# Performance work log

Measured on AMD Instinct MI355X. Metric: run time of the kernel, lower is better.

Reference implementation:

```python
import jax, jax.numpy as jnp
import numpy as np

NUM_HEADS = 16
EMBED_DIM = 1024
LN_EPS = 1e-5


def setup_inputs() -> dict:
    key = jax.random.key(0)
    ks = jax.random.split(key, 9)
    B, S, D = 4, 1024, EMBED_DIM
    return {
        "query": jax.random.normal(ks[0], (B, S, D), dtype=jnp.float32),
        "key": jax.random.normal(ks[1], (B, S, D), dtype=jnp.float32),
        "value": jax.random.normal(ks[2], (B, S, D), dtype=jnp.float32),
        "W_query": 0.01 * jax.random.normal(ks[3], (D, D), dtype=jnp.float32),
        "W_key": 0.01 * jax.random.normal(ks[4], (D, D), dtype=jnp.float32),
        "W_value": 0.01 * jax.random.normal(ks[5], (D, D), dtype=jnp.float32),
        "W_output": 0.01 * jax.random.normal(ks[6], (D, D), dtype=jnp.float32),
        "ln_gamma": jnp.ones((D,), dtype=jnp.float32),
        "ln_beta": jnp.zeros((D,), dtype=jnp.float32),
        "mask": 1,
    }


def _split_heads(x):
    # [B,S,D] -> [H,B,S,d]; torch split(dim=-1)+stack(dim=0) gives head h = cols h*d:(h+1)*d
    B, S, D = x.shape
    d = D // NUM_HEADS
    return jnp.moveaxis(x.reshape(B, S, NUM_HEADS, d), 2, 0)


def reference(query, key, value, W_query, W_key, W_value, W_output, ln_gamma, ln_beta, mask):
    B, S, D = query.shape
    d = D // NUM_HEADS
    q = _split_heads(query @ W_query)   # [H,B,S,d]
    k = _split_heads(key @ W_key)       # [H,B,S,d]
    v = _split_heads(value @ W_value)   # [H,B,S,d]
    scale = jnp.asarray(np.sqrt(d), dtype=q.dtype)
    scores = jnp.einsum("hbqd,hbkd->hbqk", q, k) / scale  # [H,B,S,S]
    attn = jax.nn.softmax(scores, axis=-1)
    if mask:
        # post-hoc causal: zero strict upper triangle, then renormalize rows
        tri = jnp.tril(jnp.ones((S, S), dtype=bool))
        attn = jnp.where(tri, attn, 0.0)
        attn = attn / jnp.sum(attn, axis=-1, keepdims=True)
    ws = jnp.einsum("hbqk,hbkd->hbqd", attn, v)            # [H,B,S,d]
    concat = jnp.moveaxis(ws, 0, 2).reshape(B, S, D)       # [B,S,D]
    out = concat @ W_output + query                        # residual
    mu = jnp.mean(out, axis=-1, keepdims=True)
    var = jnp.var(out, axis=-1, keepdims=True)
    out = (out - mu) / jnp.sqrt(var + LN_EPS) * ln_gamma + ln_beta
    return out, attn
```

## Files before the change

kernel.cpp:

```cpp
#include <hip/hip_runtime.h>
#include <hip/hip_bf16.h>

#define Bn   4
#define Sn   1024
#define Dn   1024
#define Hn   16
#define dHn  64
#define HB   (Hn * Bn)
#define MROWS (Bn * Sn)
#define QNE  ((size_t)Bn * Sn * Dn)

typedef __attribute__((ext_vector_type(8))) short bf16x8;
typedef __attribute__((ext_vector_type(4))) float f32x4;

__device__ __forceinline__ ushort f2bf(float x) {
  union { float f; unsigned u; } v; v.f = x;
  unsigned r = v.u + 0x7FFF + ((v.u >> 16) & 1);
  return (ushort)(r >> 16);
}
__device__ __forceinline__ float bf2f(ushort u) {
  union { unsigned u; float f; } v; v.u = ((unsigned)u) << 16; return v.f;
}

__device__ __forceinline__ void load_lds16(const void* g, void* l) {
  __builtin_amdgcn_global_load_lds(
      (const __attribute__((address_space(1))) unsigned int*)g,
      (__attribute__((address_space(3))) unsigned int*)l, 16, 0, 0);
}

__global__ __launch_bounds__(256) void cast3_kernel(
    const float* __restrict__ q, const float* __restrict__ k,
    const float* __restrict__ v, ushort* __restrict__ outb) {
  const float* in = blockIdx.y == 0 ? q : (blockIdx.y == 1 ? k : v);
  ushort* out = outb + (size_t)blockIdx.y * QNE;
  int idx = blockIdx.x * 256 + threadIdx.x;
  float4 x = *(const float4*)&in[(size_t)idx * 4];
  ushort4 o;
  o.x = f2bf(x.x); o.y = f2bf(x.y); o.z = f2bf(x.z); o.w = f2bf(x.w);
  *(ushort4*)&out[(size_t)idx * 4] = o;
}

__global__ __launch_bounds__(256) void transpose4_kernel(
    const float* __restrict__ Wq, const float* __restrict__ Wk,
    const float* __restrict__ Wv, const float* __restrict__ Wo,
    ushort* __restrict__ WTb) {
  const int z = blockIdx.z;
  const float* W = z == 0 ? Wq : (z == 1 ? Wk : (z == 2 ? Wv : Wo));
  ushort* WT = WTb + (size_t)z * Dn * Dn;
  __shared__ ushort T[64 * 72];
  const int k0 = blockIdx.y * 64, n0 = blockIdx.x * 64;
  const int t = threadIdx.x;
  const int r = t >> 4, c4 = (t & 15) * 4;
#pragma unroll
  for (int i = 0; i < 4; ++i) {
    int row = r + i * 16;
    float4 v = *(const float4*)&W[(size_t)(k0 + row) * Dn + n0 + c4];
    T[(c4 + 0) * 72 + row] = f2bf(v.x);
    T[(c4 + 1) * 72 + row] = f2bf(v.y);
    T[(c4 + 2) * 72 + row] = f2bf(v.z);
    T[(c4 + 3) * 72 + row] = f2bf(v.w);
  }
  __syncthreads();
#pragma unroll
  for (int i = 0; i < 2; ++i) {
    int c = t + i * 256;
    int n = c >> 3, kg = (c & 7) * 8;
    *(ulonglong2*)&WT[(size_t)(n0 + n) * Dn + k0 + kg] =
        *(const ulonglong2*)&T[n * 72 + kg];
  }
}

__global__ __launch_bounds__(256, 3) void qkv_gemm(
    const ushort* __restrict__ Ab, const ushort* __restrict__ Bb,
    ushort* __restrict__ Cb) {
  const int z = blockIdx.z;
  const ushort* A  = Ab + (size_t)z * QNE;
  const ushort* Bt = Bb + (size_t)z * Dn * Dn;
  ushort* C        = Cb + (size_t)z * QNE;
  const int M = MROWS, N = Dn, K = Dn;

  __shared__ ushort lds[17408];
  ushort* As = lds;
  ushort* Bs = lds + 4096;
  const int t = threadIdx.x;
  const int w = t >> 6, lane = t & 63;
  const int wr = (w >> 1) * 64, wc = (w & 1) * 64;
  const int l16 = lane & 15, quad = lane >> 4;
  const int m0 = blockIdx.y * 128, n0 = blockIdx.x * 128;
  const int srow = (lane >> 2);
  const int scol = (lane & 3) * 8;
  f32x4 acc[4][4] = {};
  for (int k0 = 0; k0 < K; k0 += 32) {
#pragma unroll
    for (int c = 0; c < 2; ++c) {
      int row = w * 32 + c * 16 + srow;
      load_lds16(&A[(size_t)(m0 + row) * K + k0 + scol],
                 &As[(size_t)w * 1024 + c * 512]);
      load_lds16(&Bt[(size_t)(n0 + row) * K + k0 + scol],
                 &Bs[(size_t)w * 1024 + c * 512]);
    }
    __syncthreads();
    bf16x8 af[4], bfr[4];
#pragma unroll
    for (int mi = 0; mi < 4; ++mi)
      af[mi] = *(const bf16x8*)&As[(wr + mi * 16 + l16) * 32 + quad * 8];
#pragma unroll
    for (int ni = 0; ni < 4; ++ni)
      bfr[ni] = *(const bf16x8*)&Bs[(wc + ni * 16 + l16) * 32 + quad * 8];
#pragma unroll
    for (int mi = 0; mi < 4; ++mi)
#pragma unroll
      for (int ni = 0; ni < 4; ++ni)
        acc[mi][ni] = __builtin_amdgcn_mfma_f32_16x16x32_bf16(
            af[mi], bfr[ni], acc[mi][ni], 0, 0, 0);
    __syncthreads();
  }
  if (z == 2) {
#pragma unroll
    for (int mi = 0; mi < 4; ++mi) {
      int mb = m0 + wr + mi * 16 + quad * 4;
      int b = mb >> 10, s = mb & 1023;
#pragma unroll
      for (int ni = 0; ni < 4; ++ni) {
        int n = n0 + wc + ni * 16 + l16;
        ushort4 o;
        o.x = f2bf(acc[mi][ni][0]);
        o.y = f2bf(acc[mi][ni][1]);
        o.z = f2bf(acc[mi][ni][2]);
        o.w = f2bf(acc[mi][ni][3]);
        *(ushort4*)&C[((size_t)b * N + n) * Sn + s] = o;
      }
    }
  } else {
    ushort* Cs = lds;
#pragma unroll
    for (int mi = 0; mi < 4; ++mi)
#pragma unroll
      for (int ni = 0; ni < 4; ++ni) {
        int col = wc + ni * 16 + l16;
#pragma unroll
        for (int r = 0; r < 4; ++r)
          Cs[(wr + mi * 16 + quad * 4 + r) * 136 + col] = f2bf(acc[mi][ni][r]);
      }
    __syncthreads();
#pragma unroll
    for (int i = 0; i < 8; ++i) {
      int c = t + i * 256;
      int row = c >> 4, cg = (c & 15) * 8;
      *(ulonglong2*)&C[(size_t)(m0 + row) * N + n0 + cg] =
          *(const ulonglong2*)&Cs[row * 136 + cg];
    }
  }
}

__global__ __launch_bounds__(256) void gemm_out(
    const ushort* __restrict__ A, const ushort* __restrict__ Bt,
    const float* __restrict__ resid, float* __restrict__ C,
    int M, int N, int K) {
  __shared__ ushort lds[8192];
  ushort* As = lds;
  ushort* Bs = lds + 4096;
  const int t = threadIdx.x;
  const int w = t >> 6, lane = t & 63;
  const int wr = (w >> 1) * 64, wc = (w & 1) * 64;
  const int l16 = lane & 15, quad = lane >> 4;
  const int m0 = blockIdx.y * 128, n0 = blockIdx.x * 128;
  const int srow = (lane >> 2);
  const int scol = (lane & 3) * 8;
  f32x4 acc[4][4] = {};
  for (int k0 = 0; k0 < K; k0 += 32) {
#pragma unroll
    for (int c = 0; c < 2; ++c) {
      int row = w * 32 + c * 16 + srow;
      load_lds16(&A[(size_t)(m0 + row) * K + k0 + scol],
                 &As[(size_t)w * 1024 + c * 512]);
      load_lds16(&Bt[(size_t)(n0 + row) * K + k0 + scol],
                 &Bs[(size_t)w * 1024 + c * 512]);
    }
    __syncthreads();
    bf16x8 af[4], bfr[4];
#pragma unroll
    for (int mi = 0; mi < 4; ++mi)
      af[mi] = *(const bf16x8*)&As[(wr + mi * 16 + l16) * 32 + quad * 8];
#pragma unroll
    for (int ni = 0; ni < 4; ++ni)
      bfr[ni] = *(const bf16x8*)&Bs[(wc + ni * 16 + l16) * 32 + quad * 8];
#pragma unroll
    for (int mi = 0; mi < 4; ++mi)
#pragma unroll
      for (int ni = 0; ni < 4; ++ni)
        acc[mi][ni] = __builtin_amdgcn_mfma_f32_16x16x32_bf16(
            af[mi], bfr[ni], acc[mi][ni], 0, 0, 0);
    __syncthreads();
  }
#pragma unroll
  for (int mi = 0; mi < 4; ++mi)
#pragma unroll
    for (int ni = 0; ni < 4; ++ni) {
      int n = n0 + wc + ni * 16 + l16;
#pragma unroll
      for (int r = 0; r < 4; ++r) {
        int m = m0 + wr + mi * 16 + quad * 4 + r;
        float v = acc[mi][ni][r];
        v += resid[(size_t)m * N + n];
        C[(size_t)m * N + n] = v;
      }
    }
}

__global__ __launch_bounds__(256, 3) void attn_fused(
    const ushort* __restrict__ Qp, const ushort* __restrict__ Kp,
    const ushort* __restrict__ Vt, float* __restrict__ attn,
    ushort* __restrict__ Cc) {
  const int hb = blockIdx.x, qt = blockIdx.y;
  const int h = hb >> 2, b = hb & 3;
  const int q0 = qt * 64;
  const int nkt = (qt >> 1) + 1;

  __shared__ ushort Ks[128 * 72];
  __shared__ ushort Vs[64 * 136];
  __shared__ ushort Ps[64 * 136];

  const int t = threadIdx.x;
  const int w = t >> 6, lane = t & 63;
  const int l16 = lane & 15, quad = lane >> 4;

  for (int ktz = nkt; ktz < 8; ++ktz) {
    const int k0 = ktz * 128;
#pragma unroll
    for (int i = 0; i < 4; ++i) {
      int cc = t + i * 256;
      int row = cc >> 4, cg = (cc & 15) * 8;
      float* dst = &attn[((size_t)hb * Sn + q0 + row) * Sn + k0 + cg];
      *(float4*)&dst[0] = make_float4(0.f, 0.f, 0.f, 0.f);
      *(float4*)&dst[4] = make_float4(0.f, 0.f, 0.f, 0.f);
    }
  }

  bf16x8 aq[2];
#pragma unroll
  for (int ks = 0; ks < 2; ++ks)
    aq[ks] = *(const bf16x8*)&Qp[((size_t)b * Sn + q0 + w * 16 + l16) * Dn +
                                 h * dHn + ks * 32 + quad * 8];

  float m_run[4], l_run[4];
#pragma unroll
  for (int r = 0; r < 4; ++r) { m_run[r] = -3e38f; l_run[r] = 0.f; }

  for (int kt = 0; kt < nkt; ++kt) {
    const int k0 = kt * 128;
#pragma unroll
    for (int i = 0; i < 4; ++i) {
      int cc = t + i * 256;
      int row = cc >> 3, cg = (cc & 7) * 8;
      *(ulonglong2*)&Ks[row * 72 + cg] =
          *(const ulonglong2*)&Kp[((size_t)b * Sn + k0 + row) * Dn + h * dHn + cg];
    }
    __syncthreads();
    f32x4 s[8];
#pragma unroll
    for (int ni = 0; ni < 8; ++ni) {
      f32x4 a = {};
#pragma unroll
      for (int ks = 0; ks < 2; ++ks) {
        bf16x8 bk = *(const bf16x8*)&Ks[(ni * 16 + l16) * 72 + ks * 32 + quad * 8];
        a = __builtin_amdgcn_mfma_f32_16x16x32_bf16(aq[ks], bk, a, 0, 0, 0);
      }
      s[ni] = a;
    }
    float tmax[4] = {-3e38f, -3e38f, -3e38f, -3e38f};
#pragma unroll
    for (int ni = 0; ni < 8; ++ni)
#pragma unroll
      for (int r = 0; r < 4; ++r) {
        int kg = k0 + ni * 16 + l16;
        int qg = q0 + w * 16 + quad * 4 + r;
        float v = (kg <= qg) ? s[ni][r] * 0.125f : -3e38f;
        s[ni][r] = v;
        tmax[r] = fmaxf(tmax[r], v);
      }
#pragma unroll
    for (int d = 1; d < 16; d <<= 1)
#pragma unroll
      for (int r = 0; r < 4; ++r)
        tmax[r] = fmaxf(tmax[r], __shfl_xor(tmax[r], d));
    float mnew[4], tsum[4] = {0.f, 0.f, 0.f, 0.f};
#pragma unroll
    for (int r = 0; r < 4; ++r) mnew[r] = fmaxf(m_run[r], tmax[r]);
#pragma unroll
    for (int ni = 0; ni < 8; ++ni)
#pragma unroll
      for (int r = 0; r < 4; ++r) tsum[r] += __expf(s[ni][r] - mnew[r]);
#pragma unroll
    for (int d = 1; d < 16; d <<= 1)
#pragma unroll
      for (int r = 0; r < 4; ++r) tsum[r] += __shfl_xor(tsum[r], d);
#pragma unroll
    for (int r = 0; r < 4; ++r) {
      l_run[r] = l_run[r] * __expf(m_run[r] - mnew[r]) + tsum[r];
      m_run[r] = mnew[r];
    }
    __syncthreads();
  }
  float inv_l[4];
#pragma unroll
  for (int r = 0; r < 4; ++r) inv_l[r] = 1.0f / l_run[r];

  f32x4 acc_o[4] = {};
  for (int kt = 0; kt < nkt; ++kt) {
    const int k0 = kt * 128;
#pragma unroll
    for (int i = 0; i < 4; ++i) {
      int cc = t + i * 256;
      int row = cc >> 3, cg = (cc & 7) * 8;
      *(ulonglong2*)&Ks[row * 72 + cg] =
          *(const ulonglong2*)&Kp[((size_t)b * Sn + k0 + row) * Dn + h * dHn + cg];
    }
#pragma unroll
    for (int i = 0; i < 4; ++i) {
      int cc = t + i * 256;
      int row = cc >> 4, cg = (cc & 15) * 8;
      *(ulonglong2*)&Vs[row * 136 + cg] =
          *(const ulonglong2*)&Vt[((size_t)b * Dn + h * dHn + row) * Sn + k0 + cg];
    }
    __syncthreads();
    f32x4 s[8];
#pragma unroll
    for (int ni = 0; ni < 8; ++ni) {
      f32x4 a = {};
#pragma unroll
      for (int ks = 0; ks < 2; ++ks) {
        bf16x8 bk = *(const bf16x8*)&Ks[(ni * 16 + l16) * 72 + ks * 32 + quad * 8];
        a = __builtin_amdgcn_mfma_f32_16x16x32_bf16(aq[ks], bk, a, 0, 0, 0);
      }
      s[ni] = a;
    }
#pragma unroll
    for (int ni = 0; ni < 8; ++ni)
#pragma unroll
      for (int r = 0; r < 4; ++r) {
        int kg = k0 + ni * 16 + l16;
        int qg = q0 + w * 16 + quad * 4 + r;
        float v = (kg <= qg) ? s[ni][r] * 0.125f : -3e38f;
        float p = __expf(v - m_run[r]) * inv_l[r];
        Ps[(w * 16 + quad * 4 + r) * 136 + ni * 16 + l16] = f2bf(p);
      }
#pragma unroll
    for (int ks = 0; ks < 4; ++ks) {
      bf16x8 ap = *(const bf16x8*)&Ps[(w * 16 + l16) * 136 + ks * 32 + quad * 8];
#pragma unroll
      for (int ni = 0; ni < 4; ++ni) {
        bf16x8 bv = *(const bf16x8*)&Vs[(ni * 16 + l16) * 136 + ks * 32 + quad * 8];
        acc_o[ni] = __builtin_amdgcn_mfma_f32_16x16x32_bf16(ap, bv, acc_o[ni], 0, 0, 0);
      }
    }
    __syncthreads();
#pragma unroll
    for (int i = 0; i < 4; ++i) {
      int cc = t + i * 256;
      int row = cc >> 4, cg = (cc & 15) * 8;
      bf16x8 pv = *(const bf16x8*)&Ps[row * 136 + cg];
      float* dst = &attn[((size_t)hb * Sn + q0 + row) * Sn + k0 + cg];
      *(float4*)&dst[0] = make_float4(bf2f((ushort)pv[0]), bf2f((ushort)pv[1]),
                                      bf2f((ushort)pv[2]), bf2f((ushort)pv[3]));
      *(float4*)&dst[4] = make_float4(bf2f((ushort)pv[4]), bf2f((ushort)pv[5]),
                                      bf2f((ushort)pv[6]), bf2f((ushort)pv[7]));
    }
  }
#pragma unroll
  for (int ni = 0; ni < 4; ++ni)
#pragma unroll
    for (int r = 0; r < 4; ++r) {
      int q = q0 + w * 16 + quad * 4 + r;
      int j = ni * 16 + l16;
      Cc[((size_t)b * Sn + q) * Dn + h * dHn + j] = f2bf(acc_o[ni][r]);
    }
}

__global__ __launch_bounds__(256) void ln_kernel(
    float* __restrict__ out, const float* __restrict__ gamma,
    const float* __restrict__ beta) {
  const int row = blockIdx.x;
  float* p = out + (size_t)row * Dn;
  const int t = threadIdx.x;
  float v[4];
  float s = 0.f, s2 = 0.f;
#pragma unroll
  for (int i = 0; i < 4; ++i) {
    v[i] = p[t + i * 256];
    s += v[i];
    s2 += v[i] * v[i];
  }
  __shared__ float r1[256], r2[256];
  r1[t] = s; r2[t] = s2;
  __syncthreads();
  for (int st = 128; st > 0; st >>= 1) {
    if (t < st) { r1[t] += r1[t + st]; r2[t] += r2[t + st]; }
    __syncthreads();
  }
  const float mu  = r1[0] * (1.0f / Dn);
  const float var = r2[0] * (1.0f / Dn) - mu * mu;
  const float rstd = rsqrtf(var + 1e-5f);
#pragma unroll
  for (int i = 0; i < 4; ++i) {
    int c = t + i * 256;
    p[c] = (v[i] - mu) * rstd * gamma[c] + beta[c];
  }
}

extern "C" void kernel_launch(void* const* d_in, const int* in_sizes, int n_in,
                              void* d_out, int out_size, void* d_ws, size_t ws_size,
                              hipStream_t stream) {
  const float* q_in  = (const float*)d_in[0];
  const float* k_in  = (const float*)d_in[1];
  const float* v_in  = (const float*)d_in[2];
  const float* Wq    = (const float*)d_in[3];
  const float* Wk    = (const float*)d_in[4];
  const float* Wv    = (const float*)d_in[5];
  const float* Wo    = (const float*)d_in[6];
  const float* gamma = (const float*)d_in[7];
  const float* beta  = (const float*)d_in[8];

  float* out  = (float*)d_out;
  float* attn = out + (size_t)Bn * Sn * Dn;

  ushort* ws  = (ushort*)d_ws;
  ushort* qbf = ws;
  ushort* kbf = qbf + QNE;
  ushort* vbf = kbf + QNE;
  ushort* WqT = vbf + QNE;
  ushort* WkT = WqT + (size_t)Dn * Dn;
  ushort* WvT = WkT + (size_t)Dn * Dn;
  ushort* WoT = WvT + (size_t)Dn * Dn;
  ushort* Qp  = WoT + (size_t)Dn * Dn;
  ushort* Kp  = Qp + QNE;
  ushort* Vt  = Kp + QNE;
  ushort* Cc  = Vt + QNE;

  (void)kbf; (void)vbf; (void)WkT; (void)WvT; (void)Kp;

  cast3_kernel<<<dim3(QNE / 1024, 3), 256, 0, stream>>>(q_in, k_in, v_in, qbf);
  transpose4_kernel<<<dim3(Dn / 64, Dn / 64, 4), 256, 0, stream>>>(Wq, Wk, Wv, Wo, WqT);

  qkv_gemm<<<dim3(Dn / 128, MROWS / 128, 3), 256, 0, stream>>>(qbf, WqT, Qp);

  attn_fused<<<dim3(HB, Sn / 64), 256, 0, stream>>>(Qp, Kp, Vt, attn, Cc);

  gemm_out<<<dim3(Dn / 128, MROWS / 128), 256, 0, stream>>>(Cc, WoT, q_in, out, MROWS, Dn, Dn);
  ln_kernel<<<MROWS, 256, 0, stream>>>(out, gamma, beta);
}
```

Measured before the change: 464.4 us.

## Skip masked half tiles, swizzle GEMM block order, stage V transpose, vectorize layernorm

Several independent changes land together. In the attention kernel, the last key tile for even query tiles is only half live under the causal mask, so only half of K and V are loaded and only half of the MFMAs run there. Both GEMMs remap block indices so consecutive blocks walk down M for a fixed N column, aiming for better L2 reuse of weights. The transposed V store is staged through LDS to get coalesced 16-byte writes, and layernorm switches to float4 loads with wavefront shuffle reductions instead of a shared-memory tree. These add index arithmetic and branches in exchange for less wasted work and memory traffic.

```diff
diff --git a/kernel.cpp b/kernel.cpp
--- a/kernel.cpp
+++ b/kernel.cpp
@@ -77,7 +77,7 @@
   const ushort* A  = Ab + (size_t)z * QNE;
   const ushort* Bt = Bb + (size_t)z * Dn * Dn;
   ushort* C        = Cb + (size_t)z * QNE;
-  const int M = MROWS, N = Dn, K = Dn;
+  const int N = Dn, K = Dn;
 
   __shared__ ushort lds[17408];
   ushort* As = lds;
@@ -86,7 +86,9 @@
   const int w = t >> 6, lane = t & 63;
   const int wr = (w >> 1) * 64, wc = (w & 1) * 64;
   const int l16 = lane & 15, quad = lane >> 4;
-  const int m0 = blockIdx.y * 128, n0 = blockIdx.x * 128;
+  const int flat = blockIdx.y * 8 + blockIdx.x;
+  const int nf = (flat & 7) * 32 + (flat >> 3);
+  const int m0 = (nf >> 3) * 128, n0 = (nf & 7) * 128;
   const int srow = (lane >> 2);
   const int scol = (lane & 3) * 8;
   f32x4 acc[4][4] = {};
@@ -116,20 +118,24 @@
     __syncthreads();
   }
   if (z == 2) {
-#pragma unroll
-    for (int mi = 0; mi < 4; ++mi) {
-      int mb = m0 + wr + mi * 16 + quad * 4;
-      int b = mb >> 10, s = mb & 1023;
+    ushort* Cs = lds;
+#pragma unroll
+    for (int mi = 0; mi < 4; ++mi)
 #pragma unroll
       for (int ni = 0; ni < 4; ++ni) {
-        int n = n0 + wc + ni * 16 + l16;
-        ushort4 o;
-        o.x = f2bf(acc[mi][ni][0]);
-        o.y = f2bf(acc[mi][ni][1]);
-        o.z = f2bf(acc[mi][ni][2]);
-        o.w = f2bf(acc[mi][ni][3]);
-        *(ushort4*)&C[((size_t)b * N + n) * Sn + s] = o;
-      }
+        int col = wc + ni * 16 + l16;
+#pragma unroll
+        for (int r = 0; r < 4; ++r)
+          Cs[col * 136 + wr + mi * 16 + quad * 4 + r] = f2bf(acc[mi][ni][r]);
+      }
+    __syncthreads();
+    const int b = m0 >> 10, s0 = m0 & 1023;
+#pragma unroll
+    for (int i = 0; i < 8; ++i) {
+      int c = t + i * 256;
+      int nl = c >> 4, mg = (c & 15) * 8;
+      *(ulonglong2*)&C[((size_t)b * Dn + n0 + nl) * Sn + s0 + mg] =
+          *(const ulonglong2*)&Cs[nl * 136 + mg];
     }
   } else {
     ushort* Cs = lds;
@@ -164,7 +170,9 @@
   const int w = t >> 6, lane = t & 63;
   const int wr = (w >> 1) * 64, wc = (w & 1) * 64;
   const int l16 = lane & 15, quad = lane >> 4;
-  const int m0 = blockIdx.y * 128, n0 = blockIdx.x * 128;
+  const int flat = blockIdx.y * 8 + blockIdx.x;
+  const int nf = (flat & 7) * 32 + (flat >> 3);
+  const int m0 = (nf >> 3) * 128, n0 = (nf & 7) * 128;
   const int srow = (lane >> 2);
   const int scol = (lane & 3) * 8;
   f32x4 acc[4][4] = {};
@@ -249,36 +257,45 @@
 
   for (int kt = 0; kt < nkt; ++kt) {
     const int k0 = kt * 128;
+    const bool halfT = (kt == nkt - 1) && ((qt & 1) == 0);
+    const int nni = halfT ? 4 : 8;
+    const int kiters = halfT ? 2 : 4;
 #pragma unroll
     for (int i = 0; i < 4; ++i) {
-      int cc = t + i * 256;
-      int row = cc >> 3, cg = (cc & 7) * 8;
-      *(ulonglong2*)&Ks[row * 72 + cg] =
-          *(const ulonglong2*)&Kp[((size_t)b * Sn + k0 + row) * Dn + h * dHn + cg];
+      if (i < kiters) {
+        int cc = t + i * 256;
+        int row = cc >> 3, cg = (cc & 7) * 8;
+        *(ulonglong2*)&Ks[row * 72 + cg] =
+            *(const ulonglong2*)&Kp[((size_t)b * Sn + k0 + row) * Dn + h * dHn + cg];
+      }
     }
     __syncthreads();
     f32x4 s[8];
 #pragma unroll
     for (int ni = 0; ni < 8; ++ni) {
-      f32x4 a = {};
-#pragma unroll
-      for (int ks = 0; ks < 2; ++ks) {
-        bf16x8 bk = *(const bf16x8*)&Ks[(ni * 16 + l16) * 72 + ks * 32 + quad * 8];
-        a = __builtin_amdgcn_mfma_f32_16x16x32_bf16(aq[ks], bk, a, 0, 0, 0);
-      }
-      s[ni] = a;
+      if (ni < nni) {
+        f32x4 a = {};
+#pragma unroll
+        for (int ks = 0; ks < 2; ++ks) {
+          bf16x8 bk = *(const bf16x8*)&Ks[(ni * 16 + l16) * 72 + ks * 32 + quad * 8];
+          a = __builtin_amdgcn_mfma_f32_16x16x32_bf16(aq[ks], bk, a, 0, 0, 0);
+        }
+        s[ni] = a;
+      }
     }
     float tmax[4] = {-3e38f, -3e38f, -3e38f, -3e38f};
 #pragma unroll
-    for (int ni = 0; ni < 8; ++ni)
-#pragma unroll
-      for (int r = 0; r < 4; ++r) {
-        int kg = k0 + ni * 16 + l16;
-        int qg = q0 + w * 16 + quad * 4 + r;
-        float v = (kg <= qg) ? s[ni][r] * 0.125f : -3e38f;
-        s[ni][r] = v;
-        tmax[r] = fmaxf(tmax[r], v);
-      }
+    for (int ni = 0; ni < 8; ++ni) {
+      if (ni < nni)
+#pragma unroll
+        for (int r = 0; r < 4; ++r) {
+          int kg = k0 + ni * 16 + l16;
+          int qg = q0 + w * 16 + quad * 4 + r;
+          float v = (kg <= qg) ? s[ni][r] * 0.125f : -3e38f;
+          s[ni][r] = v;
+          tmax[r] = fmaxf(tmax[r], v);
+        }
+    }
 #pragma unroll
     for (int d = 1; d < 16; d <<= 1)
 #pragma unroll
@@ -288,9 +305,11 @@
 #pragma unroll
     for (int r = 0; r < 4; ++r) mnew[r] = fmaxf(m_run[r], tmax[r]);
 #pragma unroll
-    for (int ni = 0; ni < 8; ++ni)
-#pragma unroll
-      for (int r = 0; r < 4; ++r) tsum[r] += __expf(s[ni][r] - mnew[r]);
+    for (int ni = 0; ni < 8; ++ni) {
+      if (ni < nni)
+#pragma unroll
+        for (int r = 0; r < 4; ++r) tsum[r] += __expf(s[ni][r] - mnew[r]);
+    }
 #pragma unroll
     for (int d = 1; d < 16; d <<= 1)
 #pragma unroll
@@ -309,49 +328,68 @@
   f32x4 acc_o[4] = {};
   for (int kt = 0; kt < nkt; ++kt) {
     const int k0 = kt * 128;
+    const bool halfT = (kt == nkt - 1) && ((qt & 1) == 0);
+    const int nni = halfT ? 4 : 8;
+    const int kiters = halfT ? 2 : 4;
+    const int nks = halfT ? 2 : 4;
 #pragma unroll
     for (int i = 0; i < 4; ++i) {
-      int cc = t + i * 256;
-      int row = cc >> 3, cg = (cc & 7) * 8;
-      *(ulonglong2*)&Ks[row * 72 + cg] =
-          *(const ulonglong2*)&Kp[((size_t)b * Sn + k0 + row) * Dn + h * dHn + cg];
+      if (i < kiters) {
+        int cc = t + i * 256;
+        int row = cc >> 3, cg = (cc & 7) * 8;
+        *(ulonglong2*)&Ks[row * 72 + cg] =
+            *(const ulonglong2*)&Kp[((size_t)b * Sn + k0 + row) * Dn + h * dHn + cg];
+      }
     }
 #pragma unroll
     for (int i = 0; i < 4; ++i) {
-      int cc = t + i * 256;
-      int row = cc >> 4, cg = (cc & 15) * 8;
-      *(ulonglong2*)&Vs[row * 136 + cg] =
-          *(const ulonglong2*)&Vt[((size_t)b * Dn + h * dHn + row) * Sn + k0 + cg];
+      if (i < 2 * kiters) {
+        int cc = t + i * 256;
+        int row, cg;
+        if (halfT) { row = cc >> 3; cg = (cc & 7) * 8; }
+        else       { row = cc >> 4; cg = (cc & 15) * 8; }
+        *(ulonglong2*)&Vs[row * 136 + cg] =
+            *(const ulonglong2*)&Vt[((size_t)b * Dn + h * dHn + row) * Sn + k0 + cg];
+      }
     }
     __syncthreads();
     f32x4 s[8];
 #pragma unroll
     for (int ni = 0; ni < 8; ++ni) {
-      f32x4 a = {};
-#pragma unroll
-      for (int ks = 0; ks < 2; ++ks) {
-        bf16x8 bk = *(const bf16x8*)&Ks[(ni * 16 + l16) * 72 + ks * 32 + quad * 8];
-        a = __builtin_amdgcn_mfma_f32_16x16x32_bf16(aq[ks], bk, a, 0, 0, 0);
-      }
-      s[ni] = a;
+      if (ni < nni) {
+        f32x4 a = {};
+#pragma unroll
+        for (int ks = 0; ks < 2; ++ks) {
+          bf16x8 bk = *(const bf16x8*)&Ks[(ni * 16 + l16) * 72 + ks * 32 + quad * 8];
+          a = __builtin_amdgcn_mfma_f32_16x16x32_bf16(aq[ks], bk, a, 0, 0, 0);
+        }
+        s[ni] = a;
+      }
     }
 #pragma unroll
     for (int ni = 0; ni < 8; ++ni)
 #pragma unroll
       for (int r = 0; r < 4; ++r) {
-        int kg = k0 + ni * 16 + l16;
-        int qg = q0 + w * 16 + quad * 4 + r;
-        float v = (kg <= qg) ? s[ni][r] * 0.125f : -3e38f;
-        float p = __expf(v - m_run[r]) * inv_l[r];
+        float p;
+        if (ni < nni) {
+          int kg = k0 + ni * 16 + l16;
+          int qg = q0 + w * 16 + quad * 4 + r;
+          float v = (kg <= qg) ? s[ni][r] * 0.125f : -3e38f;
+          p = __expf(v - m_run[r]) * inv_l[r];
+        } else {
+          p = 0.f;
+        }
         Ps[(w * 16 + quad * 4 + r) * 136 + ni * 16 + l16] = f2bf(p);
       }
 #pragma unroll
     for (int ks = 0; ks < 4; ++ks) {
-      bf16x8 ap = *(const bf16x8*)&Ps[(w * 16 + l16) * 136 + ks * 32 + quad * 8];
-#pragma unroll
-      for (int ni = 0; ni < 4; ++ni) {
-        bf16x8 bv = *(const bf16x8*)&Vs[(ni * 16 + l16) * 136 + ks * 32 + quad * 8];
-        acc_o[ni] = __builtin_amdgcn_mfma_f32_16x16x32_bf16(ap, bv, acc_o[ni], 0, 0, 0);
+      if (ks < nks) {
+        bf16x8 ap = *(const bf16x8*)&Ps[(w * 16 + l16) * 136 + ks * 32 + quad * 8];
+#pragma unroll
+        for (int ni = 0; ni < 4; ++ni) {
+          bf16x8 bv = *(const bf16x8*)&Vs[(ni * 16 + l16) * 136 + ks * 32 + quad * 8];
+          acc_o[ni] = __builtin_amdgcn_mfma_f32_16x16x32_bf16(ap, bv, acc_o[ni], 0, 0, 0);
+        }
       }
     }
     __syncthreads();
@@ -383,29 +421,31 @@
   const int row = blockIdx.x;
   float* p = out + (size_t)row * Dn;
   const int t = threadIdx.x;
-  float v[4];
-  float s = 0.f, s2 = 0.f;
-#pragma unroll
-  for (int i = 0; i < 4; ++i) {
-    v[i] = p[t + i * 256];
-    s += v[i];
-    s2 += v[i] * v[i];
-  }
-  __shared__ float r1[256], r2[256];
-  r1[t] = s; r2[t] = s2;
+  float4 x = *(const float4*)&p[t * 4];
+  float s  = x.x + x.y + x.z + x.w;
+  float s2 = x.x * x.x + x.y * x.y + x.z * x.z + x.w * x.w;
+#pragma unroll
+  for (int d = 1; d < 64; d <<= 1) {
+    s  += __shfl_xor(s, d);
+    s2 += __shfl_xor(s2, d);
+  }
+  __shared__ float a1[4], a2[4];
+  const int w = t >> 6, lane = t & 63;
+  if (lane == 0) { a1[w] = s; a2[w] = s2; }
   __syncthreads();
-  for (int st = 128; st > 0; st >>= 1) {
-    if (t < st) { r1[t] += r1[t + st]; r2[t] += r2[t + st]; }
-    __syncthreads();
-  }
-  const float mu  = r1[0] * (1.0f / Dn);
-  const float var = r2[0] * (1.0f / Dn) - mu * mu;
+  s  = a1[0] + a1[1] + a1[2] + a1[3];
+  s2 = a2[0] + a2[1] + a2[2] + a2[3];
+  const float mu  = s * (1.0f / Dn);
+  const float var = s2 * (1.0f / Dn) - mu * mu;
   const float rstd = rsqrtf(var + 1e-5f);
-#pragma unroll
-  for (int i = 0; i < 4; ++i) {
-    int c = t + i * 256;
-    p[c] = (v[i] - mu) * rstd * gamma[c] + beta[c];
-  }
+  float4 g  = *(const float4*)&gamma[t * 4];
+  float4 be = *(const float4*)&beta[t * 4];
+  float4 o;
+  o.x = (x.x - mu) * rstd * g.x + be.x;
+  o.y = (x.y - mu) * rstd * g.y + be.y;
+  o.z = (x.z - mu) * rstd * g.z + be.z;
+  o.w = (x.w - mu) * rstd * g.w + be.w;
+  *(float4*)&p[t * 4] = o;
 }
 
 extern "C" void kernel_launch(void* const* d_in, const int* in_sizes, int n_in,
```

New measurement: 462.3 us. About the same (-0.5%).
